# Optimization experiments

Hardware: AMD Instinct MI355X
Metric: run time of the kernel (lower is better)

## Reference

```python
import jax, jax.numpy as jnp
import numpy as np

D_MODEL = 1024
NUM_HEADS = 16
THETA = 10000.0
NEG = -1000000.0  # masked_fill value used by the torch code


def _rope(x, token_positions, theta):
    # x: [B, H, S, d_head]; token_positions: [S] int
    d_k = x.shape[-1]
    half = d_k // 2
    j = jnp.arange(half, dtype=jnp.float32)
    inv_freq = theta ** (-(2.0 * j) / d_k)                      # [half]
    ang = token_positions.astype(jnp.float32)[:, None] * inv_freq  # [S, half]
    cos = jnp.cos(ang)
    sin = jnp.sin(ang)
    xp = x.reshape(x.shape[:-1] + (half, 2))  # adjacent pairs (pc, 2)
    x0, x1 = xp[..., 0], xp[..., 1]
    o0 = x0 * cos - x1 * sin
    o1 = x0 * sin + x1 * cos
    out = jnp.stack([o0, o1], axis=-1)
    return out.reshape(x.shape)


def setup_inputs() -> dict:
    key = jax.random.key(0)
    k0, k1, k2 = jax.random.split(key, 3)
    B, S, D = 2, 2048, D_MODEL
    std = (2.0 / (D + D)) ** 0.5
    X = jax.random.normal(k0, (B, S, D), dtype=jnp.float32)
    QKV_weights = jax.random.normal(k1, (3 * D, D), dtype=jnp.float32) * std
    O_weights = jax.random.normal(k2, (D, D), dtype=jnp.float32) * std
    token_positions = jnp.arange(S, dtype=jnp.int32)
    return {"X": X, "token_positions": token_positions,
            "QKV_weights": QKV_weights, "O_weights": O_weights}


def reference(X, token_positions, QKV_weights, O_weights):
    B, S, D = X.shape
    H = NUM_HEADS
    dh = D // H
    qkv = jnp.einsum('od,bsd->bso', QKV_weights, X)  # [B, S, 3D]
    Q, K, V = jnp.split(qkv, 3, axis=-1)

    def split_heads(t):
        return t.reshape(B, S, H, dh).transpose(0, 2, 1, 3)  # [B,H,S,dh]

    Q, K, V = split_heads(Q), split_heads(K), split_heads(V)
    Q = _rope(Q, token_positions, THETA)
    K = _rope(K, token_positions, THETA)

    scores = (jnp.einsum('bhqd,bhkd->bhqk', Q, K) / jnp.sqrt(jnp.float32(dh))).astype(jnp.float32)
    causal = jnp.tril(jnp.ones((S, S), dtype=bool))
    scores = jnp.where(causal, scores, NEG)
    probs = jax.nn.softmax(scores, axis=-1)
    attn = jnp.einsum('bhqk,bhkd->bhqd', probs, V.astype(jnp.float32)).astype(Q.dtype)
    attn = attn.transpose(0, 2, 1, 3).reshape(B, S, D)
    return jnp.einsum('od,bsd->bso', O_weights, attn)
```

## Files before the change

### kernel.cpp

```cpp
#include <hip/hip_runtime.h>
#include <math.h>

#define S_LEN 2048

using bf16x8  = __attribute__((ext_vector_type(8))) short;
using shortx4 = __attribute__((ext_vector_type(4))) short;
using f32x4   = __attribute__((ext_vector_type(4))) float;

static __device__ __forceinline__ short f2bf(float f) {
  unsigned u = __float_as_uint(f);
  u += 0x7fffu + ((u >> 16) & 1u);
  return (short)(u >> 16);
}
static __device__ __forceinline__ float bf2f(short s) {
  return __uint_as_float(((unsigned)(unsigned short)s) << 16);
}

#define GLD_LDS16(gptr, lptr)                                                  \
  __builtin_amdgcn_global_load_lds(                                            \
      (__attribute__((address_space(1))) void*)(gptr),                         \
      (__attribute__((address_space(3))) void*)(lptr), 16, 0, 0)

#define EXP2_SHIFT 20.0f

static __device__ __forceinline__ f32x4 exp2s4(f32x4 a) {
  return (f32x4){__builtin_amdgcn_exp2f(a[0] - EXP2_SHIFT),
                 __builtin_amdgcn_exp2f(a[1] - EXP2_SHIFT),
                 __builtin_amdgcn_exp2f(a[2] - EXP2_SHIFT),
                 __builtin_amdgcn_exp2f(a[3] - EXP2_SHIFT)};
}

__global__ void rope_table_kernel(const int* __restrict__ tok, float2* __restrict__ table) {
  int i = blockIdx.x * blockDim.x + threadIdx.x;
  if (i >= S_LEN * 32) return;
  int s = i >> 5, j = i & 31;
  double pos = (double)tok[s];
  double ang = pos * pow(10000.0, -(double)j / 32.0);
  table[i] = make_float2((float)cos(ang), (float)sin(ang));
}

__global__ __launch_bounds__(256) void cvt_bf16_kernel(const float* __restrict__ X,
                                                       const float* __restrict__ W1,
                                                       const float* __restrict__ W2,
                                                       short* __restrict__ Xb,
                                                       short* __restrict__ W1b,
                                                       short* __restrict__ W2b) {
  size_t idx = (size_t)(blockIdx.x * 256 + threadIdx.x) * 8;
  const float* src;
  short* dst;
  size_t off;
  if (idx < 4194304) { src = X; dst = Xb; off = idx; }
  else if (idx < 4194304 + 3145728) { src = W1; dst = W1b; off = idx - 4194304; }
  else { src = W2; dst = W2b; off = idx - (4194304 + 3145728); }
  float4 a = *(const float4*)(src + off);
  float4 b = *(const float4*)(src + off + 4);
  bf16x8 o = {f2bf(a.x), f2bf(a.y), f2bf(a.z), f2bf(a.w),
              f2bf(b.x), f2bf(b.y), f2bf(b.z), f2bf(b.w)};
  *(bf16x8*)(dst + off) = o;
}

template <int BM, typename OutT>
__global__ __launch_bounds__(256) void gemm_ll(const short* __restrict__ A,
                                               const short* __restrict__ B,
                                               OutT* __restrict__ C,
                                               int M, int N, int K) {
  constexpr int MI = BM / 32;
  constexpr int AI = BM / 64;
  __shared__ short As[BM * 32];
  __shared__ short Bs[128 * 32];
  const int tid  = threadIdx.x;
  const int lane = tid & 63;
  const int wv   = tid >> 6;
  const int wm   = (wv >> 1) * (BM / 2);
  const int wn   = (wv & 1) * 64;
  const int m16  = lane & 15;
  const int q4   = lane >> 4;
  const int rowBase = blockIdx.y * BM;
  const int colBase = blockIdx.x * 128;
  const int lrow = lane >> 2;
  const int lseg = lane & 3;

  f32x4 acc[MI][4];
#pragma unroll
  for (int i = 0; i < MI; ++i)
#pragma unroll
    for (int j = 0; j < 4; ++j) acc[i][j] = (f32x4){0.f, 0.f, 0.f, 0.f};

  const short* Agl = A + (size_t)rowBase * K;
  const short* Bgl = B + (size_t)colBase * K;

  for (int kk = 0; kk < K; kk += 32) {
#pragma unroll
    for (int i = 0; i < AI; ++i) {
      const int r0 = (wv * AI + i) * 16;
      GLD_LDS16(Agl + (size_t)(r0 + lrow) * K + kk + lseg * 8, &As[r0 * 32]);
    }
#pragma unroll
    for (int i = 0; i < 2; ++i) {
      const int r0 = (wv * 2 + i) * 16;
      GLD_LDS16(Bgl + (size_t)(r0 + lrow) * K + kk + lseg * 8, &Bs[r0 * 32]);
    }
    __syncthreads();

    bf16x8 af[MI], bfv[4];
#pragma unroll
    for (int mi = 0; mi < MI; ++mi)
      af[mi] = *(const bf16x8*)&As[(wm + mi * 16 + m16) * 32 + q4 * 8];
#pragma unroll
    for (int ni = 0; ni < 4; ++ni)
      bfv[ni] = *(const bf16x8*)&Bs[(wn + ni * 16 + m16) * 32 + q4 * 8];
#pragma unroll
    for (int mi = 0; mi < MI; ++mi)
#pragma unroll
      for (int ni = 0; ni < 4; ++ni)
        acc[mi][ni] = __builtin_amdgcn_mfma_f32_16x16x32_bf16(af[mi], bfv[ni], acc[mi][ni], 0, 0, 0);
    __syncthreads();
  }

#pragma unroll
  for (int mi = 0; mi < MI; ++mi)
#pragma unroll
    for (int ni = 0; ni < 4; ++ni) {
      const int rbase = rowBase + wm + mi * 16 + q4 * 4;
      const int cidx  = colBase + wn + ni * 16 + m16;
#pragma unroll
      for (int r = 0; r < 4; ++r) {
        float v = acc[mi][ni][r];
        if constexpr (sizeof(OutT) == 2)
          C[(size_t)(rbase + r) * N + cidx] = (OutT)f2bf(v);
        else
          C[(size_t)(rbase + r) * N + cidx] = (OutT)v;
      }
    }
}

__global__ __launch_bounds__(256) void prep_kernel(const short* __restrict__ qkvb,
                                                   const float2* __restrict__ table,
                                                   short* __restrict__ Qb,
                                                   short* __restrict__ Kb,
                                                   short* __restrict__ VT) {
  __shared__ __align__(16) short VtL[64 * 72];
  const int tid = threadIdx.x;
  const int st  = blockIdx.x, bh = blockIdx.y;
  const int b   = bh >> 4, h = bh & 15;
  const int r   = tid >> 2, seg = tid & 3;
  const int s   = st * 64 + r;
  const int pr  = (r & 15) * 4 + (r >> 4);
  const short* base = qkvb + (size_t)(b * S_LEN + s) * 3072 + h * 64 + seg * 16;
  const float QSCALE = 0.125f * 1.44269504f;

#pragma unroll
  for (int which = 0; which < 2; ++which) {
    const short* src = base + which * 1024;
    short in[16], ob[16];
    *(bf16x8*)&in[0] = ((const bf16x8*)src)[0];
    *(bf16x8*)&in[8] = ((const bf16x8*)src)[1];
#pragma unroll
    for (int p = 0; p < 8; ++p) {
      float x0 = bf2f(in[2 * p]), x1 = bf2f(in[2 * p + 1]);
      float2 cs = table[s * 32 + seg * 8 + p];
      float o0 = x0 * cs.x - x1 * cs.y;
      float o1 = x0 * cs.y + x1 * cs.x;
      if (which == 0) { o0 *= QSCALE; o1 *= QSCALE; }
      ob[2 * p]     = f2bf(o0);
      ob[2 * p + 1] = f2bf(o1);
    }
    short* dst = (which ? Kb : Qb) + ((size_t)bh * S_LEN + s) * 64 + seg * 16;
    ((bf16x8*)dst)[0] = *(bf16x8*)&ob[0];
    ((bf16x8*)dst)[1] = *(bf16x8*)&ob[8];
  }

  {
    const short* vsrc = base + 2048;
    short in[16];
    *(bf16x8*)&in[0] = ((const bf16x8*)vsrc)[0];
    *(bf16x8*)&in[8] = ((const bf16x8*)vsrc)[1];
#pragma unroll
    for (int d = 0; d < 16; ++d)
      VtL[(seg * 16 + d) * 72 + pr] = in[d];
  }
  __syncthreads();
  short* vdst = VT + ((size_t)bh * 64 + r) * S_LEN + st * 64 + seg * 16;
  ((bf16x8*)vdst)[0] = *(bf16x8*)&VtL[r * 72 + seg * 16];
  ((bf16x8*)vdst)[1] = *(bf16x8*)&VtL[r * 72 + seg * 16 + 8];
}

__global__ __launch_bounds__(256, 2) void attn_mfma(const short* __restrict__ Qb,
                                                    const short* __restrict__ Kb,
                                                    const short* __restrict__ VT,
                                                    short* __restrict__ attnb) {
  __shared__ __align__(16) short Ks[64 * 72];
  __shared__ __align__(16) short Vs[64 * 72];
  __shared__ __align__(16) short Ps[64 * 72];
  const int tid  = threadIdx.x;
  const int lane = tid & 63;
  const int w    = tid >> 6;
  const int m16  = lane & 15;
  const int quad = lane >> 4;
  const int bh   = blockIdx.y;
  const int pair = blockIdx.x;
  const int b    = bh >> 4, h = bh & 15;
  const short* Qh = Qb + (size_t)bh * S_LEN * 64;
  const short* Kh = Kb + (size_t)bh * S_LEN * 64;
  const short* Vh = VT + (size_t)bh * 64 * S_LEN;

  const int srow = tid >> 2;
  const int seg  = tid & 3;

  const bf16x8 ones = {16256, 16256, 16256, 16256, 16256, 16256, 16256, 16256};

  for (int half = 0; half < 2; ++half) {
    const int jt = half ? (31 - pair) : pair;
    const int q0 = jt * 64;
    const int ktiles = jt + 1;

    bf16x8 qf[2];
#pragma unroll
    for (int ks = 0; ks < 2; ++ks)
      qf[ks] = *(const bf16x8*)(Qh + (size_t)(q0 + w * 16 + m16) * 64 + ks * 32 + quad * 8);

    f32x4 O[4], Lacc;
#pragma unroll
    for (int c = 0; c < 4; ++c) O[c] = (f32x4){0.f, 0.f, 0.f, 0.f};
    Lacc = (f32x4){0.f, 0.f, 0.f, 0.f};

    bf16x8 kst[2], vst[2];
    {
      const short* kg = Kh + (size_t)srow * 64 + seg * 16;
      const short* vg = Vh + (size_t)srow * S_LEN + seg * 16;
      kst[0] = ((const bf16x8*)kg)[0]; kst[1] = ((const bf16x8*)kg)[1];
      vst[0] = ((const bf16x8*)vg)[0]; vst[1] = ((const bf16x8*)vg)[1];
    }

    for (int t = 0; t < ktiles; ++t) {
      {
        bf16x8* kd = (bf16x8*)&Ks[srow * 72 + seg * 16];
        kd[0] = kst[0]; kd[1] = kst[1];
        bf16x8* vd = (bf16x8*)&Vs[srow * 72 + seg * 16];
        vd[0] = vst[0]; vd[1] = vst[1];
      }
      __syncthreads();

      if (t + 1 < ktiles) {
        const short* kg = Kh + (size_t)((t + 1) * 64 + srow) * 64 + seg * 16;
        const short* vg = Vh + (size_t)srow * S_LEN + (t + 1) * 64 + seg * 16;
        kst[0] = ((const bf16x8*)kg)[0]; kst[1] = ((const bf16x8*)kg)[1];
        vst[0] = ((const bf16x8*)vg)[0]; vst[1] = ((const bf16x8*)vg)[1];
      }

      f32x4 sc[4];
#pragma unroll
      for (int c = 0; c < 4; ++c) sc[c] = (f32x4){0.f, 0.f, 0.f, 0.f};
#pragma unroll
      for (int ks = 0; ks < 2; ++ks) {
#pragma unroll
        for (int c = 0; c < 4; ++c) {
          bf16x8 kf = *(const bf16x8*)&Ks[(c * 16 + m16) * 72 + ks * 32 + quad * 8];
          sc[c] = __builtin_amdgcn_mfma_f32_16x16x32_bf16(qf[ks], kf, sc[c], 0, 0, 0);
        }
      }

      if (t == jt) {
#pragma unroll
        for (int c = 0; c < 4; ++c) {
          const int kin = c * 16 + m16;
#pragma unroll
          for (int rr = 0; rr < 4; ++rr) {
            const int rloc = w * 16 + quad * 4 + rr;
            if (kin > rloc) sc[c][rr] = -1e30f;
          }
        }
      }

#pragma unroll
      for (int c = 0; c < 4; ++c) sc[c] = exp2s4(sc[c]);
#pragma unroll
      for (int rr = 0; rr < 4; ++rr) {
        shortx4 pk = {f2bf(sc[0][rr]), f2bf(sc[1][rr]), f2bf(sc[2][rr]), f2bf(sc[3][rr])};
        *(shortx4*)&Ps[(w * 16 + quad * 4 + rr) * 72 + m16 * 4] = pk;
      }

#pragma unroll
      for (int ks = 0; ks < 2; ++ks) {
        bf16x8 pa = *(const bf16x8*)&Ps[(w * 16 + m16) * 72 + ks * 32 + quad * 8];
#pragma unroll
        for (int c = 0; c < 4; ++c) {
          bf16x8 vb = *(const bf16x8*)&Vs[(c * 16 + m16) * 72 + ks * 32 + quad * 8];
          O[c] = __builtin_amdgcn_mfma_f32_16x16x32_bf16(pa, vb, O[c], 0, 0, 0);
        }
        Lacc = __builtin_amdgcn_mfma_f32_16x16x32_bf16(pa, ones, Lacc, 0, 0, 0);
      }
      __syncthreads();
    }

    float inv[4];
#pragma unroll
    for (int rr = 0; rr < 4; ++rr) inv[rr] = __frcp_rn(Lacc[rr]);
#pragma unroll
    for (int c = 0; c < 4; ++c) {
      const int col = h * 64 + c * 16 + m16;
#pragma unroll
      for (int rr = 0; rr < 4; ++rr) {
        const int q = q0 + w * 16 + quad * 4 + rr;
        attnb[(size_t)(b * S_LEN + q) * 1024 + col] = f2bf(O[c][rr] * inv[rr]);
      }
    }
  }
}

extern "C" void kernel_launch(void* const* d_in, const int* in_sizes, int n_in,
                              void* d_out, int out_size, void* d_ws, size_t ws_size,
                              hipStream_t stream) {
  const float* X    = (const float*)d_in[0];
  const int*   tok  = (const int*)d_in[1];
  const float* Wqkv = (const float*)d_in[2];
  const float* Wo   = (const float*)d_in[3];
  float* out = (float*)d_out;

  char* w = (char*)d_ws;
  float2* table = (float2*)w;
  short*  qkvb  = (short*)(w + 524288);
  short*  Qb    = (short*)(w + 524288 + 25165824);
  short*  Kb    = Qb + 4194304;
  short*  VTt   = Kb + 4194304;
  short*  Xb    = VTt + 4194304;
  short*  Wqkvb = Xb + 4194304;
  short*  Wob   = Wqkvb + 3145728;
  short*  attnb = qkvb;

  hipLaunchKernelGGL(rope_table_kernel, dim3(256), dim3(256), 0, stream, tok, table);
  hipLaunchKernelGGL(cvt_bf16_kernel, dim3(4096), dim3(256), 0, stream,
                     X, Wqkv, Wo, Xb, Wqkvb, Wob);
  hipLaunchKernelGGL((gemm_ll<128, short>), dim3(24, 32), dim3(256), 0, stream,
                     Xb, Wqkvb, qkvb, 4096, 3072, 1024);
  hipLaunchKernelGGL(prep_kernel, dim3(32, 32), dim3(256), 0, stream,
                     qkvb, table, Qb, Kb, VTt);
  hipLaunchKernelGGL(attn_mfma, dim3(16, 32), dim3(256), 0, stream,
                     Qb, Kb, VTt, attnb);
  hipLaunchKernelGGL((gemm_ll<64, float>), dim3(8, 64), dim3(256), 0, stream,
                     attnb, Wob, out, 4096, 1024, 1024);
}
```

Measured before the change: 193.7 us.

## Enlarge attention query tile to 128 rows and merge init kernels

The attention kernel now has each block handle 128 query rows (32 per wave as two 16-row MFMA tiles) instead of processing two 64-row tiles, so every K/V tile loaded into LDS feeds twice as much MFMA work. The grid becomes 32 heads by 16 query tiles, ordered largest-causal-work first, and an extra barrier is added after the P write. The rope table and bf16 conversion kernels are merged into one launch to save a kernel launch. In exchange, register use and LDS grow, and the causal load balancing that came from pairing tiles is lost.

```diff
diff --git a/kernel.cpp b/kernel.cpp
--- a/kernel.cpp
+++ b/kernel.cpp
@@ -30,33 +30,34 @@
                  __builtin_amdgcn_exp2f(a[3] - EXP2_SHIFT)};
 }
 
-__global__ void rope_table_kernel(const int* __restrict__ tok, float2* __restrict__ table) {
-  int i = blockIdx.x * blockDim.x + threadIdx.x;
-  if (i >= S_LEN * 32) return;
-  int s = i >> 5, j = i & 31;
-  double pos = (double)tok[s];
-  double ang = pos * pow(10000.0, -(double)j / 32.0);
-  table[i] = make_float2((float)cos(ang), (float)sin(ang));
-}
-
-__global__ __launch_bounds__(256) void cvt_bf16_kernel(const float* __restrict__ X,
-                                                       const float* __restrict__ W1,
-                                                       const float* __restrict__ W2,
-                                                       short* __restrict__ Xb,
-                                                       short* __restrict__ W1b,
-                                                       short* __restrict__ W2b) {
-  size_t idx = (size_t)(blockIdx.x * 256 + threadIdx.x) * 8;
-  const float* src;
-  short* dst;
-  size_t off;
-  if (idx < 4194304) { src = X; dst = Xb; off = idx; }
-  else if (idx < 4194304 + 3145728) { src = W1; dst = W1b; off = idx - 4194304; }
-  else { src = W2; dst = W2b; off = idx - (4194304 + 3145728); }
-  float4 a = *(const float4*)(src + off);
-  float4 b = *(const float4*)(src + off + 4);
-  bf16x8 o = {f2bf(a.x), f2bf(a.y), f2bf(a.z), f2bf(a.w),
-              f2bf(b.x), f2bf(b.y), f2bf(b.z), f2bf(b.w)};
-  *(bf16x8*)(dst + off) = o;
+__global__ __launch_bounds__(256) void init_kernel(const float* __restrict__ X,
+                                                   const float* __restrict__ W1,
+                                                   const float* __restrict__ W2,
+                                                   const int* __restrict__ tok,
+                                                   short* __restrict__ Xb,
+                                                   short* __restrict__ W1b,
+                                                   short* __restrict__ W2b,
+                                                   float2* __restrict__ table) {
+  if (blockIdx.x < 4096) {
+    size_t idx = (size_t)(blockIdx.x * 256 + threadIdx.x) * 8;
+    const float* src;
+    short* dst;
+    size_t off;
+    if (idx < 4194304) { src = X; dst = Xb; off = idx; }
+    else if (idx < 4194304 + 3145728) { src = W1; dst = W1b; off = idx - 4194304; }
+    else { src = W2; dst = W2b; off = idx - (4194304 + 3145728); }
+    float4 a = *(const float4*)(src + off);
+    float4 b = *(const float4*)(src + off + 4);
+    bf16x8 o = {f2bf(a.x), f2bf(a.y), f2bf(a.z), f2bf(a.w),
+                f2bf(b.x), f2bf(b.y), f2bf(b.z), f2bf(b.w)};
+    *(bf16x8*)(dst + off) = o;
+  } else {
+    int i = (blockIdx.x - 4096) * 256 + threadIdx.x;
+    int s = i >> 5, j = i & 31;
+    double pos = (double)tok[s];
+    double ang = pos * pow(10000.0, -(double)j / 32.0);
+    table[i] = make_float2((float)cos(ang), (float)sin(ang));
+  }
 }
 
 template <int BM, typename OutT>
@@ -191,118 +192,142 @@
                                                     short* __restrict__ attnb) {
   __shared__ __align__(16) short Ks[64 * 72];
   __shared__ __align__(16) short Vs[64 * 72];
-  __shared__ __align__(16) short Ps[64 * 72];
+  __shared__ __align__(16) short Ps[128 * 72];
   const int tid  = threadIdx.x;
   const int lane = tid & 63;
   const int w    = tid >> 6;
   const int m16  = lane & 15;
   const int quad = lane >> 4;
-  const int bh   = blockIdx.y;
-  const int pair = blockIdx.x;
+  const int bh   = blockIdx.x;
+  const int jt   = 15 - blockIdx.y;
   const int b    = bh >> 4, h = bh & 15;
   const short* Qh = Qb + (size_t)bh * S_LEN * 64;
   const short* Kh = Kb + (size_t)bh * S_LEN * 64;
   const short* Vh = VT + (size_t)bh * 64 * S_LEN;
 
-  const int srow = tid >> 2;
-  const int seg  = tid & 3;
+  const int srow = tid >> 3;
+  const int seg  = tid & 7;
 
   const bf16x8 ones = {16256, 16256, 16256, 16256, 16256, 16256, 16256, 16256};
 
-  for (int half = 0; half < 2; ++half) {
-    const int jt = half ? (31 - pair) : pair;
-    const int q0 = jt * 64;
-    const int ktiles = jt + 1;
-
-    bf16x8 qf[2];
+  const int q0 = jt * 128;
+  const int ktiles = 2 * jt + 2;
+
+  bf16x8 qf[2][2];
+#pragma unroll
+  for (int m = 0; m < 2; ++m)
 #pragma unroll
     for (int ks = 0; ks < 2; ++ks)
-      qf[ks] = *(const bf16x8*)(Qh + (size_t)(q0 + w * 16 + m16) * 64 + ks * 32 + quad * 8);
-
-    f32x4 O[4], Lacc;
-#pragma unroll
-    for (int c = 0; c < 4; ++c) O[c] = (f32x4){0.f, 0.f, 0.f, 0.f};
-    Lacc = (f32x4){0.f, 0.f, 0.f, 0.f};
-
-    bf16x8 kst[2], vst[2];
+      qf[m][ks] = *(const bf16x8*)(Qh + (size_t)(q0 + w * 32 + m * 16 + m16) * 64 + ks * 32 + quad * 8);
+
+  f32x4 O[2][4], Lacc[2];
+#pragma unroll
+  for (int m = 0; m < 2; ++m) {
+    Lacc[m] = (f32x4){0.f, 0.f, 0.f, 0.f};
+#pragma unroll
+    for (int c = 0; c < 4; ++c) O[m][c] = (f32x4){0.f, 0.f, 0.f, 0.f};
+  }
+
+  bf16x8 kst[2], vst[2];
+#pragma unroll
+  for (int i = 0; i < 2; ++i) {
+    kst[i] = *(const bf16x8*)(Kh + (size_t)(i * 32 + srow) * 64 + seg * 8);
+    vst[i] = *(const bf16x8*)(Vh + (size_t)(i * 32 + srow) * S_LEN + seg * 8);
+  }
+
+  for (int t = 0; t < ktiles; ++t) {
     {
-      const short* kg = Kh + (size_t)srow * 64 + seg * 16;
-      const short* vg = Vh + (size_t)srow * S_LEN + seg * 16;
-      kst[0] = ((const bf16x8*)kg)[0]; kst[1] = ((const bf16x8*)kg)[1];
-      vst[0] = ((const bf16x8*)vg)[0]; vst[1] = ((const bf16x8*)vg)[1];
-    }
-
-    for (int t = 0; t < ktiles; ++t) {
-      {
-        bf16x8* kd = (bf16x8*)&Ks[srow * 72 + seg * 16];
-        kd[0] = kst[0]; kd[1] = kst[1];
-        bf16x8* vd = (bf16x8*)&Vs[srow * 72 + seg * 16];
-        vd[0] = vst[0]; vd[1] = vst[1];
-      }
-      __syncthreads();
-
-      if (t + 1 < ktiles) {
-        const short* kg = Kh + (size_t)((t + 1) * 64 + srow) * 64 + seg * 16;
-        const short* vg = Vh + (size_t)srow * S_LEN + (t + 1) * 64 + seg * 16;
-        kst[0] = ((const bf16x8*)kg)[0]; kst[1] = ((const bf16x8*)kg)[1];
-        vst[0] = ((const bf16x8*)vg)[0]; vst[1] = ((const bf16x8*)vg)[1];
-      }
-
-      f32x4 sc[4];
-#pragma unroll
-      for (int c = 0; c < 4; ++c) sc[c] = (f32x4){0.f, 0.f, 0.f, 0.f};
-#pragma unroll
-      for (int ks = 0; ks < 2; ++ks) {
+#pragma unroll
+      for (int i = 0; i < 2; ++i) {
+        *(bf16x8*)&Ks[(i * 32 + srow) * 72 + seg * 8] = kst[i];
+        *(bf16x8*)&Vs[(i * 32 + srow) * 72 + seg * 8] = vst[i];
+      }
+    }
+    __syncthreads();
+
+    if (t + 1 < ktiles) {
+#pragma unroll
+      for (int i = 0; i < 2; ++i) {
+        kst[i] = *(const bf16x8*)(Kh + (size_t)((t + 1) * 64 + i * 32 + srow) * 64 + seg * 8);
+        vst[i] = *(const bf16x8*)(Vh + (size_t)(i * 32 + srow) * S_LEN + (t + 1) * 64 + seg * 8);
+      }
+    }
+
+    f32x4 sc[2][4];
+#pragma unroll
+    for (int m = 0; m < 2; ++m)
+#pragma unroll
+      for (int c = 0; c < 4; ++c) sc[m][c] = (f32x4){0.f, 0.f, 0.f, 0.f};
+#pragma unroll
+    for (int ks = 0; ks < 2; ++ks) {
+#pragma unroll
+      for (int c = 0; c < 4; ++c) {
+        bf16x8 kf = *(const bf16x8*)&Ks[(c * 16 + m16) * 72 + ks * 32 + quad * 8];
+#pragma unroll
+        for (int m = 0; m < 2; ++m)
+          sc[m][c] = __builtin_amdgcn_mfma_f32_16x16x32_bf16(qf[m][ks], kf, sc[m][c], 0, 0, 0);
+      }
+    }
+
+    if (t >= ktiles - 2) {
+#pragma unroll
+      for (int m = 0; m < 2; ++m)
 #pragma unroll
         for (int c = 0; c < 4; ++c) {
-          bf16x8 kf = *(const bf16x8*)&Ks[(c * 16 + m16) * 72 + ks * 32 + quad * 8];
-          sc[c] = __builtin_amdgcn_mfma_f32_16x16x32_bf16(qf[ks], kf, sc[c], 0, 0, 0);
-        }
-      }
-
-      if (t == jt) {
-#pragma unroll
-        for (int c = 0; c < 4; ++c) {
-          const int kin = c * 16 + m16;
+          const int kg = t * 64 + c * 16 + m16;
 #pragma unroll
           for (int rr = 0; rr < 4; ++rr) {
-            const int rloc = w * 16 + quad * 4 + rr;
-            if (kin > rloc) sc[c][rr] = -1e30f;
+            const int qg = q0 + w * 32 + m * 16 + quad * 4 + rr;
+            if (kg > qg) sc[m][c][rr] = -1e30f;
           }
         }
-      }
-
-#pragma unroll
-      for (int c = 0; c < 4; ++c) sc[c] = exp2s4(sc[c]);
+    }
+
+#pragma unroll
+    for (int m = 0; m < 2; ++m) {
+#pragma unroll
+      for (int c = 0; c < 4; ++c) sc[m][c] = exp2s4(sc[m][c]);
 #pragma unroll
       for (int rr = 0; rr < 4; ++rr) {
-        shortx4 pk = {f2bf(sc[0][rr]), f2bf(sc[1][rr]), f2bf(sc[2][rr]), f2bf(sc[3][rr])};
-        *(shortx4*)&Ps[(w * 16 + quad * 4 + rr) * 72 + m16 * 4] = pk;
-      }
-
-#pragma unroll
-      for (int ks = 0; ks < 2; ++ks) {
-        bf16x8 pa = *(const bf16x8*)&Ps[(w * 16 + m16) * 72 + ks * 32 + quad * 8];
-#pragma unroll
-        for (int c = 0; c < 4; ++c) {
-          bf16x8 vb = *(const bf16x8*)&Vs[(c * 16 + m16) * 72 + ks * 32 + quad * 8];
-          O[c] = __builtin_amdgcn_mfma_f32_16x16x32_bf16(pa, vb, O[c], 0, 0, 0);
-        }
-        Lacc = __builtin_amdgcn_mfma_f32_16x16x32_bf16(pa, ones, Lacc, 0, 0, 0);
-      }
-      __syncthreads();
-    }
-
+        shortx4 pk = {f2bf(sc[m][0][rr]), f2bf(sc[m][1][rr]),
+                      f2bf(sc[m][2][rr]), f2bf(sc[m][3][rr])};
+        *(shortx4*)&Ps[(w * 32 + m * 16 + quad * 4 + rr) * 72 + m16 * 4] = pk;
+      }
+    }
+    __syncthreads();
+
+#pragma unroll
+    for (int ks = 0; ks < 2; ++ks) {
+      bf16x8 pa[2];
+#pragma unroll
+      for (int m = 0; m < 2; ++m)
+        pa[m] = *(const bf16x8*)&Ps[(w * 32 + m * 16 + m16) * 72 + ks * 32 + quad * 8];
+#pragma unroll
+      for (int c = 0; c < 4; ++c) {
+        bf16x8 vb = *(const bf16x8*)&Vs[(c * 16 + m16) * 72 + ks * 32 + quad * 8];
+#pragma unroll
+        for (int m = 0; m < 2; ++m)
+          O[m][c] = __builtin_amdgcn_mfma_f32_16x16x32_bf16(pa[m], vb, O[m][c], 0, 0, 0);
+      }
+#pragma unroll
+      for (int m = 0; m < 2; ++m)
+        Lacc[m] = __builtin_amdgcn_mfma_f32_16x16x32_bf16(pa[m], ones, Lacc[m], 0, 0, 0);
+    }
+    __syncthreads();
+  }
+
+#pragma unroll
+  for (int m = 0; m < 2; ++m) {
     float inv[4];
 #pragma unroll
-    for (int rr = 0; rr < 4; ++rr) inv[rr] = __frcp_rn(Lacc[rr]);
+    for (int rr = 0; rr < 4; ++rr) inv[rr] = __frcp_rn(Lacc[m][rr]);
 #pragma unroll
     for (int c = 0; c < 4; ++c) {
       const int col = h * 64 + c * 16 + m16;
 #pragma unroll
       for (int rr = 0; rr < 4; ++rr) {
-        const int q = q0 + w * 16 + quad * 4 + rr;
-        attnb[(size_t)(b * S_LEN + q) * 1024 + col] = f2bf(O[c][rr] * inv[rr]);
+        const int q = q0 + w * 32 + m * 16 + quad * 4 + rr;
+        attnb[(size_t)(b * S_LEN + q) * 1024 + col] = f2bf(O[m][c][rr] * inv[rr]);
       }
     }
   }
@@ -328,14 +353,13 @@
   short*  Wob   = Wqkvb + 3145728;
   short*  attnb = qkvb;
 
-  hipLaunchKernelGGL(rope_table_kernel, dim3(256), dim3(256), 0, stream, tok, table);
-  hipLaunchKernelGGL(cvt_bf16_kernel, dim3(4096), dim3(256), 0, stream,
-                     X, Wqkv, Wo, Xb, Wqkvb, Wob);
+  hipLaunchKernelGGL(init_kernel, dim3(4352), dim3(256), 0, stream,
+                     X, Wqkv, Wo, tok, Xb, Wqkvb, Wob, table);
   hipLaunchKernelGGL((gemm_ll<128, short>), dim3(24, 32), dim3(256), 0, stream,
                      Xb, Wqkvb, qkvb, 4096, 3072, 1024);
   hipLaunchKernelGGL(prep_kernel, dim3(32, 32), dim3(256), 0, stream,
                      qkvb, table, Qb, Kb, VTt);
-  hipLaunchKernelGGL(attn_mfma, dim3(16, 32), dim3(256), 0, stream,
+  hipLaunchKernelGGL(attn_mfma, dim3(32, 16), dim3(256), 0, stream,
                      Qb, Kb, VTt, attnb);
   hipLaunchKernelGGL((gemm_ll<64, float>), dim3(8, 64), dim3(256), 0, stream,
                      attnb, Wob, out, 4096, 1024, 1024);
```

Measured after the change: 193.9 us. About the same (+0.1%).
